# Kernel optimization log

Measured on AMD Instinct MI355X. Metric: run time of the kernel, lower is better.

## Reference

```python
import jax, jax.numpy as jnp
import numpy as np

D_MODEL = 1024
NUM_HEADS = 16
D_K = D_MODEL // NUM_HEADS
MAX_LEN = 1024
BATCH = 8
SEQ = 1024


def setup_inputs() -> dict:
    key = jax.random.key(0)
    ks = jax.random.split(key, 12)
    s = 0.02
    inp = {
        "x": jax.random.normal(ks[0], (BATCH, SEQ, D_MODEL), dtype=jnp.float32),
        "Wq": jax.random.normal(ks[1], (D_MODEL, D_MODEL), dtype=jnp.float32) * s,
        "bq": jnp.zeros((D_MODEL,), dtype=jnp.float32),
        "Wk": jax.random.normal(ks[2], (D_MODEL, D_MODEL), dtype=jnp.float32) * s,
        "bk": jnp.zeros((D_MODEL,), dtype=jnp.float32),
        "Wv": jax.random.normal(ks[3], (D_MODEL, D_MODEL), dtype=jnp.float32) * s,
        "bv": jnp.zeros((D_MODEL,), dtype=jnp.float32),
        "Wo": jax.random.normal(ks[4], (D_MODEL, D_MODEL), dtype=jnp.float32) * s,
        "bo": jnp.zeros((D_MODEL,), dtype=jnp.float32),
        "relative_k": jax.random.normal(ks[5], (2 * MAX_LEN - 1, D_K), dtype=jnp.float32),
        "relative_v": jax.random.normal(ks[6], (2 * MAX_LEN - 1, D_K), dtype=jnp.float32),
    }
    return inp


def reference(x, Wq, bq, Wk, bk, Wv, bv, Wo, bo, relative_k, relative_v):
    B, L, D = x.shape
    H, dk = NUM_HEADS, D_K
    # projections (nn.Linear: y = x @ W.T + b), split into heads -> [B,H,L,dk]
    Q = (x @ Wq.T + bq).reshape(B, L, H, dk).transpose(0, 2, 1, 3)
    K = (x @ Wk.T + bk).reshape(B, L, H, dk).transpose(0, 2, 1, 3)
    V = (x @ Wv.T + bv).reshape(B, L, H, dk).transpose(0, 2, 1, 3)
    # relative position index table: rel_pos[l, r] = r - l + max_len - 1
    rel_pos = jnp.arange(L)[None, :] - jnp.arange(L)[:, None] + (MAX_LEN - 1)
    rel_k = relative_k[rel_pos]  # [L, L, dk]
    rel_v = relative_v[rel_pos]  # [L, L, dk]
    scale = 1.0 / np.sqrt(dk).astype(np.float32)
    scores = jnp.einsum('bhld,bhrd->bhlr', Q, K) * scale
    scores = scores + jnp.einsum('bhld,lrd->bhlr', Q, rel_k)
    attn = jax.nn.softmax(scores, axis=-1)  # [B,H,L,L]
    out = jnp.einsum('bhlr,bhrd->bhld', attn, V)
    out = out + jnp.einsum('bhlr,lrd->bhld', attn, rel_v)
    out = out.transpose(0, 2, 1, 3).reshape(B, L, D)
    return out @ Wo.T + bo
```

## Files before the change

kernel.cpp:

```cpp
#include <hip/hip_runtime.h>

typedef _Float16 f16;
typedef _Float16 f16x2 __attribute__((ext_vector_type(2)));
typedef _Float16 f16x8 __attribute__((ext_vector_type(8)));
typedef float f32x4 __attribute__((ext_vector_type(4)));

static __device__ __forceinline__ f32x4 mfma16(f16x8 a, f16x8 b, f32x4 c) {
  return __builtin_amdgcn_mfma_f32_16x16x32_f16(a, b, c, 0, 0, 0);
}

#define GL16(GP, LP)                                                         \
  __builtin_amdgcn_global_load_lds(                                          \
      (const __attribute__((address_space(1))) void*)(GP),                   \
      (__attribute__((address_space(3))) void*)(LP), 16, 0, 0)

__global__ void pack_f16_kernel(const float* __restrict__ s, f16* __restrict__ d, int n) {
  int i = blockIdx.x * 256 + threadIdx.x;
  if (i < n) d[i] = (f16)s[i];
}

__global__ void pack_relk_kernel(const float* __restrict__ relk, f16* __restrict__ dst) {
  int idx = blockIdx.x * 256 + threadIdx.x;
  dst[idx] = (idx < 2047 * 64) ? (f16)relk[idx] : (f16)0.f;
}

__global__ void pack_relvt_kernel(const float* __restrict__ relv, f16* __restrict__ dst) {
  int idx = blockIdx.x * 256 + threadIdx.x;
  int dd = idx >> 11, p = idx & 2047;
  dst[idx] = (p < 2047) ? (f16)relv[p * 64 + dd] : (f16)0.f;
}

template <int OUT_F32, int BIAS_ROW>
__global__ __launch_bounds__(256, 2) void gemm_bt(
    const f16* __restrict__ A, const f16* __restrict__ B,
    const float* __restrict__ bias, void* __restrict__ Cout,
    int M, int N, int Kd, float oscale) {
  __shared__ __align__(16) f16 Al[2 * 128 * 64];
  __shared__ __align__(16) f16 Bl[2 * 128 * 64];
  const int tid = threadIdx.x;
  const int w = tid >> 6, lane = tid & 63;
  const int l15 = lane & 15, hi = lane >> 4;
  const long i0 = (long)blockIdx.y * 128, j0 = (long)blockIdx.x * 128;
  const int wr = (w >> 1) * 64, wc = (w & 1) * 64;
  const int sx = (l15 & 7) * 8;

  const int row_in = lane >> 3, c_lds = lane & 7;
  const int cg8 = (c_lds ^ row_in) * 8;
  const f16* agl = A + (i0 + w * 8 + row_in) * Kd + cg8;
  const f16* bgl = B + (j0 + w * 8 + row_in) * Kd + cg8;
  const int lbase = (w * 8) * 64;

#define GSTAGE(BUF, K0)                                          \
  do {                                                           \
    f16* al = Al + (BUF) * 8192 + lbase;                         \
    f16* bl = Bl + (BUF) * 8192 + lbase;                         \
    GL16(agl + (K0), al);                                        \
    GL16(agl + 32l * Kd + (K0), al + 32 * 64);                   \
    GL16(agl + 64l * Kd + (K0), al + 64 * 64);                   \
    GL16(agl + 96l * Kd + (K0), al + 96 * 64);                   \
    GL16(bgl + (K0), bl);                                        \
    GL16(bgl + 32l * Kd + (K0), bl + 32 * 64);                   \
    GL16(bgl + 64l * Kd + (K0), bl + 64 * 64);                   \
    GL16(bgl + 96l * Kd + (K0), bl + 96 * 64);                   \
  } while (0)

  f32x4 acc[4][4];
#pragma unroll
  for (int a = 0; a < 4; a++)
#pragma unroll
    for (int b2 = 0; b2 < 4; b2++) acc[a][b2] = (f32x4){0.f, 0.f, 0.f, 0.f};

  GSTAGE(0, 0);
  int cur = 0;
  for (int k0 = 0; k0 < Kd; k0 += 64) {
    if (k0 + 64 < Kd) {
      GSTAGE(cur ^ 1, k0 + 64);
      asm volatile("s_waitcnt vmcnt(8)" ::: "memory");
    } else {
      asm volatile("s_waitcnt vmcnt(0)" ::: "memory");
    }
    __builtin_amdgcn_s_barrier();
    __builtin_amdgcn_sched_barrier(0);
    const f16* Ac = Al + cur * 8192;
    const f16* Bc = Bl + cur * 8192;
#pragma unroll
    for (int ks = 0; ks < 2; ks++) {
      f16x8 af[4], bf[4];
#pragma unroll
      for (int mb = 0; mb < 4; mb++)
        af[mb] = *(const f16x8*)&Ac[(wr + mb * 16 + l15) * 64 + ((ks * 32 + hi * 8) ^ sx)];
#pragma unroll
      for (int nb = 0; nb < 4; nb++)
        bf[nb] = *(const f16x8*)&Bc[(wc + nb * 16 + l15) * 64 + ((ks * 32 + hi * 8) ^ sx)];
#pragma unroll
      for (int mb = 0; mb < 4; mb++)
#pragma unroll
        for (int nb = 0; nb < 4; nb++) acc[mb][nb] = mfma16(af[mb], bf[nb], acc[mb][nb]);
    }
    asm volatile("s_waitcnt lgkmcnt(0)" ::: "memory");
    __builtin_amdgcn_s_barrier();
    cur ^= 1;
  }
#undef GSTAGE
#pragma unroll
  for (int mb = 0; mb < 4; mb++) {
#pragma unroll
    for (int nb = 0; nb < 4; nb++) {
      long row = i0 + wr + mb * 16 + hi * 4;
      long col = j0 + wc + nb * 16 + l15;
      float bc = BIAS_ROW ? 0.f : bias[col];
#pragma unroll
      for (int i = 0; i < 4; i++) {
        float v = acc[mb][nb][i] + (BIAS_ROW ? bias[row + i] : bc);
        v *= oscale;
        if (OUT_F32)
          ((float*)Cout)[(row + i) * N + col] = v;
        else
          ((f16*)Cout)[(row + i) * N + col] = (f16)v;
      }
    }
  }
}

__global__ __launch_bounds__(256, 2) void attn_kernel(
    const f16* __restrict__ Qh, const f16* __restrict__ Kh,
    const f16* __restrict__ Vth, const f16* __restrict__ relKh,
    const f16* __restrict__ relVTh, f16* __restrict__ AO) {
  __shared__ __align__(16) f16 SH[38912];
  f16* const ldsK = SH;
  f16* const ldsRK = SH + 4096;
  f16* const ldsP = SH;
  f16* const ldsPS = SH + 9216;
  f16* const ldsV = SH + 22528;
  f16* const ldsRV = SH + 26624;

  const int tid = threadIdx.x;
  const int w = tid >> 6, lane = tid & 63;
  const int l15 = lane & 15, hi = lane >> 4;
  const int flat = blockIdx.x;
  const int xcd = flat & 7, slot = flat >> 3;
  const int bh = xcd * 16 + (slot >> 3);
  const int qt = slot & 7;
  const int b = bh >> 4, h = bh & 15;
  const int l0 = qt * 128;
  const int cu = 6 - 2 * w;
  const int rvco = 96 - 32 * w;
  const int sx = (l15 & 7) * 8;

  const int row_in = lane >> 3;
  const int c_lds = lane & 7;
  const int cg8 = (c_lds ^ row_in) * 8;
  const f16* kgl = Kh + ((long)(b * 1024 + w * 16 + row_in)) * 1024 + h * 64 + cg8;
  const f16* vgl = Vth + ((long)(h * 64 + w * 16 + row_in)) * 8192 + b * 1024 + cg8;
  const f16* rkgl = relKh + (long)(896 - l0 + w * 48 + row_in) * 64 + cg8;
#define RVP(Q)                                                                   \
  (relVTh + (long)(((w * 6 + (Q)) * 64 + lane) / 24) * 2048 + (896 - l0) +       \
   ((((w * 6 + (Q)) * 64 + lane) % 24) ^ ((((w * 6 + (Q)) * 64 + lane) / 24) & 7)) * 8)
  const f16* rvg0 = RVP(0);
  const f16* rvg1 = RVP(1);
  const f16* rvg2 = RVP(2);
  const f16* rvg3 = RVP(3);
  const f16* rvg4 = RVP(4);
  const f16* rvg5 = RVP(5);
#undef RVP

  const long qbase = ((long)(b * 1024 + l0 + w * 32 + l15)) * 1024 + h * 64 + hi * 8;
  const f16x8 qf00 = *(const f16x8*)(Qh + qbase);
  const f16x8 qf01 = *(const f16x8*)(Qh + qbase + 32);
  const f16x8 qf10 = *(const f16x8*)(Qh + qbase + 16l * 1024);
  const f16x8 qf11 = *(const f16x8*)(Qh + qbase + 16l * 1024 + 32);

  const f16x8 ones1 = {(f16)1.f, (f16)1.f, (f16)1.f, (f16)1.f,
                       (f16)1.f, (f16)1.f, (f16)1.f, (f16)1.f};

  f32x4 acc_o[2][4];
#pragma unroll
  for (int g = 0; g < 2; g++)
#pragma unroll
    for (int cf = 0; cf < 4; cf++) acc_o[g][cf] = (f32x4){0.f, 0.f, 0.f, 0.f};
  float mrow[2][4], lsum[2][4];
#pragma unroll
  for (int g = 0; g < 2; g++)
#pragma unroll
    for (int i = 0; i < 4; i++) {
      mrow[g][i] = -1e30f;
      lsum[g][i] = 0.f;
    }

  for (int kt = 0; kt < 16; kt++) {
    const int r0 = kt * 64;
    __syncthreads();
    {
      const long ko = (long)r0 * 1024;
      GL16(kgl + ko, ldsK + (w * 16) * 64);
      GL16(kgl + ko + 8 * 1024, ldsK + (w * 16 + 8) * 64);
      GL16(vgl + r0, ldsV + (w * 16) * 64);
      GL16(vgl + r0 + 8l * 8192, ldsV + (w * 16 + 8) * 64);
      const int rko = r0 * 64;
      GL16(rkgl + rko, ldsRK + (w * 48) * 64);
      GL16(rkgl + rko + 512, ldsRK + (w * 48 + 8) * 64);
      GL16(rkgl + rko + 1024, ldsRK + (w * 48 + 16) * 64);
      GL16(rkgl + rko + 1536, ldsRK + (w * 48 + 24) * 64);
      GL16(rkgl + rko + 2048, ldsRK + (w * 48 + 32) * 64);
      GL16(rkgl + rko + 2560, ldsRK + (w * 48 + 40) * 64);
      GL16(rvg0 + r0, ldsRV + (w * 6 + 0) * 512);
      GL16(rvg1 + r0, ldsRV + (w * 6 + 1) * 512);
      GL16(rvg2 + r0, ldsRV + (w * 6 + 2) * 512);
      GL16(rvg3 + r0, ldsRV + (w * 6 + 3) * 512);
      GL16(rvg4 + r0, ldsRV + (w * 6 + 4) * 512);
      GL16(rvg5 + r0, ldsRV + (w * 6 + 5) * 512);
    }
    __syncthreads();

    f32x4 sacc[2][4], qracc[2][5];
#pragma unroll
    for (int g = 0; g < 2; g++) {
#pragma unroll
      for (int cf = 0; cf < 4; cf++) sacc[g][cf] = (f32x4){0.f, 0.f, 0.f, 0.f};
#pragma unroll
      for (int j = 0; j < 5; j++) qracc[g][j] = (f32x4){0.f, 0.f, 0.f, 0.f};
    }
    __builtin_amdgcn_s_setprio(1);
#pragma unroll
    for (int ks = 0; ks < 2; ks++) {
      f16x8 kf[4], rf[6];
#pragma unroll
      for (int cf = 0; cf < 4; cf++)
        kf[cf] = *(const f16x8*)&ldsK[(cf * 16 + l15) * 64 + ((ks * 32 + hi * 8) ^ sx)];
#pragma unroll
      for (int j = 0; j < 6; j++)
        rf[j] =
            *(const f16x8*)&ldsRK[((cu + j) * 16 + l15) * 64 + ((ks * 32 + hi * 8) ^ sx)];
      f16x8 q0 = ks ? qf01 : qf00;
      f16x8 q1 = ks ? qf11 : qf10;
#pragma unroll
      for (int cf = 0; cf < 4; cf++) {
        sacc[0][cf] = mfma16(q0, kf[cf], sacc[0][cf]);
        sacc[1][cf] = mfma16(q1, kf[cf], sacc[1][cf]);
      }
#pragma unroll
      for (int j = 0; j < 5; j++) {
        qracc[0][j] = mfma16(q0, rf[j + 1], qracc[0][j]);
        qracc[1][j] = mfma16(q1, rf[j], qracc[1][j]);
      }
    }
    __builtin_amdgcn_s_setprio(0);
    __syncthreads();

#pragma unroll
    for (int g = 0; g < 2; g++)
#pragma unroll
      for (int i = 0; i < 4; i++) {
        int t = 15 + l15 - (hi * 4 + i);
        int idx = (hi * 16 + (t & 15)) * 4;
        bool wrap = t >= 16;
#pragma unroll
        for (int cf = 0; cf < 4; cf++) {
          auto pkv = __builtin_amdgcn_cvt_pkrtz(qracc[g][cf][i], qracc[g][cf + 1][i]);
          int gg = __builtin_amdgcn_ds_bpermute(idx, __builtin_bit_cast(int, pkv));
          f16x2 two = __builtin_bit_cast(f16x2, gg);
          sacc[g][cf][i] += (float)(wrap ? two[1] : two[0]);
        }
      }

    float rmax[2][4];
#pragma unroll
    for (int g = 0; g < 2; g++)
#pragma unroll
      for (int i = 0; i < 4; i++)
        rmax[g][i] = fmaxf(fmaxf(sacc[g][0][i], sacc[g][1][i]),
                           fmaxf(sacc[g][2][i], sacc[g][3][i]));
#pragma unroll
    for (int m = 1; m < 16; m <<= 1)
#pragma unroll
      for (int g = 0; g < 2; g++)
#pragma unroll
        for (int i = 0; i < 4; i++)
          rmax[g][i] = fmaxf(rmax[g][i], __shfl_xor(rmax[g][i], m, 64));
    {
      bool big = false;
#pragma unroll
      for (int g = 0; g < 2; g++)
#pragma unroll
        for (int i = 0; i < 4; i++) big |= rmax[g][i] > mrow[g][i] + 8.f;
      if (__any(big)) {
#pragma unroll
        for (int g = 0; g < 2; g++)
#pragma unroll
          for (int i = 0; i < 4; i++) {
            float mn = fmaxf(mrow[g][i], rmax[g][i]);
            float al = __expf(mrow[g][i] - mn);
            mrow[g][i] = mn;
            lsum[g][i] *= al;
#pragma unroll
            for (int cf = 0; cf < 4; cf++) acc_o[g][cf][i] *= al;
          }
      }
    }
#pragma unroll
    for (int g = 0; g < 2; g++)
#pragma unroll
      for (int cf = 0; cf < 4; cf++)
#pragma unroll
        for (int i = 0; i < 4; i++)
          sacc[g][cf][i] = __expf(sacc[g][cf][i] - mrow[g][i]);

    const uint4 z4 = make_uint4(0u, 0u, 0u, 0u);
#pragma unroll
    for (int r2 = 0; r2 < 2; r2++)
#pragma unroll
      for (int s = 0; s < 3; s++)
        *(uint4*)&ldsPS[(w * 32 + r2 * 16 + (lane >> 2)) * 104 + (lane & 3) * 8 + 32 * s] =
            z4;
#pragma unroll
    for (int g = 0; g < 2; g++)
#pragma unroll
      for (int cf = 0; cf < 4; cf++)
#pragma unroll
        for (int i = 0; i < 4; i++) {
          int rr = 16 * g + hi * 4 + i;
          int ri = cf * 16 + l15;
          f16 ph = (f16)sacc[g][cf][i];
          ldsP[(w * 32 + rr) * 72 + ri] = ph;
          ldsPS[(w * 32 + rr) * 104 + 31 + ri - rr] = ph;
        }
    __builtin_amdgcn_sched_barrier(0);

    __builtin_amdgcn_s_setprio(1);
    f32x4 rs0 = (f32x4){0.f, 0.f, 0.f, 0.f}, rs1 = (f32x4){0.f, 0.f, 0.f, 0.f};
#pragma unroll
    for (int ks = 0; ks < 2; ks++) {
      f16x8 pa0 = *(const f16x8*)&ldsP[(w * 32 + l15) * 72 + ks * 32 + hi * 8];
      f16x8 pa1 = *(const f16x8*)&ldsP[(w * 32 + 16 + l15) * 72 + ks * 32 + hi * 8];
      rs0 = mfma16(pa0, ones1, rs0);
      rs1 = mfma16(pa1, ones1, rs1);
#pragma unroll
      for (int cf = 0; cf < 4; cf++) {
        f16x8 vb = *(const f16x8*)&ldsV[(cf * 16 + l15) * 64 + ((ks * 32 + hi * 8) ^ sx)];
        acc_o[0][cf] = mfma16(pa0, vb, acc_o[0][cf]);
        acc_o[1][cf] = mfma16(pa1, vb, acc_o[1][cf]);
      }
    }
#pragma unroll
    for (int ks = 0; ks < 3; ks++) {
      f16x8 ps0 = *(const f16x8*)&ldsPS[(w * 32 + l15) * 104 + ks * 32 + hi * 8];
      f16x8 ps1 = *(const f16x8*)&ldsPS[(w * 32 + 16 + l15) * 104 + ks * 32 + hi * 8];
#pragma unroll
      for (int cf = 0; cf < 4; cf++) {
        f16x8 rb = *(const f16x8*)&ldsRV[(cf * 16 + l15) * 192 +
                                         ((rvco + ks * 32 + hi * 8) ^ sx)];
        acc_o[0][cf] = mfma16(ps0, rb, acc_o[0][cf]);
        acc_o[1][cf] = mfma16(ps1, rb, acc_o[1][cf]);
      }
    }
    __builtin_amdgcn_s_setprio(0);
#pragma unroll
    for (int i = 0; i < 4; i++) {
      lsum[0][i] += rs0[i];
      lsum[1][i] += rs1[i];
    }
  }
#pragma unroll
  for (int g = 0; g < 2; g++)
#pragma unroll
    for (int cf = 0; cf < 4; cf++)
#pragma unroll
      for (int i = 0; i < 4; i++) {
        float v = acc_o[g][cf][i] / lsum[g][i];
        AO[((long)(b * 1024 + l0 + w * 32 + 16 * g + hi * 4 + i)) * 1024 + h * 64 +
           cf * 16 + l15] = (f16)v;
      }
}

extern "C" void kernel_launch(void* const* d_in, const int* in_sizes, int n_in,
                              void* d_out, int out_size, void* d_ws, size_t ws_size,
                              hipStream_t stream) {
  const float* x = (const float*)d_in[0];
  const float* Wq = (const float*)d_in[1];
  const float* bq = (const float*)d_in[2];
  const float* Wk = (const float*)d_in[3];
  const float* bk = (const float*)d_in[4];
  const float* Wv = (const float*)d_in[5];
  const float* bv = (const float*)d_in[6];
  const float* Wo = (const float*)d_in[7];
  const float* bo = (const float*)d_in[8];
  const float* relk = (const float*)d_in[9];
  const float* relv = (const float*)d_in[10];
  float* out = (float*)d_out;

  char* ws = (char*)d_ws;
  size_t off = 0;
  auto alloc = [&](size_t bytes) {
    char* p = ws + off;
    off += (bytes + 255) & ~(size_t)255;
    return p;
  };
  f16* xh = (f16*)alloc(8192ull * 1024 * 2);
  f16* Wqh = (f16*)alloc(1024ull * 1024 * 2);
  f16* Wkh = (f16*)alloc(1024ull * 1024 * 2);
  f16* Wvh = (f16*)alloc(1024ull * 1024 * 2);
  f16* Woh = (f16*)alloc(1024ull * 1024 * 2);
  f16* relKh = (f16*)alloc(2048ull * 64 * 2);
  f16* relVTh = (f16*)alloc(64ull * 2048 * 2);
  f16* Qh = (f16*)alloc(8192ull * 1024 * 2);
  f16* Kh = (f16*)alloc(8192ull * 1024 * 2);
  f16* Vth = (f16*)alloc(1024ull * 8192 * 2);
  f16* AOh = (f16*)alloc(8192ull * 1024 * 2);
  if (ws_size < off) return;

  pack_f16_kernel<<<32768, 256, 0, stream>>>(x, xh, 8192 * 1024);
  pack_f16_kernel<<<4096, 256, 0, stream>>>(Wq, Wqh, 1024 * 1024);
  pack_f16_kernel<<<4096, 256, 0, stream>>>(Wk, Wkh, 1024 * 1024);
  pack_f16_kernel<<<4096, 256, 0, stream>>>(Wv, Wvh, 1024 * 1024);
  pack_f16_kernel<<<4096, 256, 0, stream>>>(Wo, Woh, 1024 * 1024);
  pack_relk_kernel<<<512, 256, 0, stream>>>(relk, relKh);
  pack_relvt_kernel<<<512, 256, 0, stream>>>(relv, relVTh);

  dim3 g1(8, 64);
  gemm_bt<0, 0><<<g1, 256, 0, stream>>>(xh, Wqh, bq, Qh, 8192, 1024, 1024, 1.0f);
  gemm_bt<0, 0><<<g1, 256, 0, stream>>>(xh, Wkh, bk, Kh, 8192, 1024, 1024, 0.125f);
  dim3 g2(64, 8);
  gemm_bt<0, 1><<<g2, 256, 0, stream>>>(Wvh, xh, bv, Vth, 1024, 8192, 1024, 1.0f);

  attn_kernel<<<1024, 256, 0, stream>>>(Qh, Kh, Vth, relKh, relVTh, AOh);

  gemm_bt<1, 0><<<g1, 256, 0, stream>>>(AOh, Woh, bo, out, 8192, 1024, 1024, 1.0f);
}
```

Measured before the change: 300.1 us.

## Fuse pack kernels, batch Q/K GEMMs, and split attention load wait

Merges the five f32-to-f16 pack launches into one vectorized float4 kernel and the two relative-table packs into one kernel. Batches the Q and K projections into a single GEMM launch using blockIdx.z to select weights, bias, output and scale. In the attention loop, V and relative-V loads are issued last and a partial vmcnt wait replaces the full __syncthreads, so the QK stage can start while those loads are still in flight. This cuts launch count and tail effects and overlaps memory with compute, but relies on hand-counted vmcnt ordering being correct.

```diff
diff --git a/kernel.cpp b/kernel.cpp
--- a/kernel.cpp
+++ b/kernel.cpp
@@ -2,6 +2,7 @@
 
 typedef _Float16 f16;
 typedef _Float16 f16x2 __attribute__((ext_vector_type(2)));
+typedef _Float16 f16x4 __attribute__((ext_vector_type(4)));
 typedef _Float16 f16x8 __attribute__((ext_vector_type(8)));
 typedef float f32x4 __attribute__((ext_vector_type(4)));
 
@@ -14,27 +15,55 @@
       (const __attribute__((address_space(1))) void*)(GP),                   \
       (__attribute__((address_space(3))) void*)(LP), 16, 0, 0)
 
-__global__ void pack_f16_kernel(const float* __restrict__ s, f16* __restrict__ d, int n) {
+__global__ void pack5_kernel(const float4* __restrict__ x, const float4* __restrict__ wq,
+                             const float4* __restrict__ wk, const float4* __restrict__ wv,
+                             const float4* __restrict__ wo, f16* __restrict__ xh,
+                             f16* __restrict__ wqh, f16* __restrict__ wkh,
+                             f16* __restrict__ wvh, f16* __restrict__ woh) {
   int i = blockIdx.x * 256 + threadIdx.x;
-  if (i < n) d[i] = (f16)s[i];
-}
-
-__global__ void pack_relk_kernel(const float* __restrict__ relk, f16* __restrict__ dst) {
+  const float4* s;
+  f16* d;
+  int off;
+  if (i < 2097152) {
+    s = x;
+    d = xh;
+    off = i;
+  } else {
+    int j = i - 2097152;
+    int seg = j >> 18;
+    off = j & 262143;
+    s = seg == 0 ? wq : seg == 1 ? wk : seg == 2 ? wv : wo;
+    d = seg == 0 ? wqh : seg == 1 ? wkh : seg == 2 ? wvh : woh;
+  }
+  float4 v = s[off];
+  f16x4 o = {(f16)v.x, (f16)v.y, (f16)v.z, (f16)v.w};
+  *(f16x4*)&d[off * 4] = o;
+}
+
+__global__ void packrel_kernel(const float* __restrict__ relk,
+                               const float* __restrict__ relv,
+                               f16* __restrict__ relKh, f16* __restrict__ relVTh) {
   int idx = blockIdx.x * 256 + threadIdx.x;
-  dst[idx] = (idx < 2047 * 64) ? (f16)relk[idx] : (f16)0.f;
-}
-
-__global__ void pack_relvt_kernel(const float* __restrict__ relv, f16* __restrict__ dst) {
-  int idx = blockIdx.x * 256 + threadIdx.x;
-  int dd = idx >> 11, p = idx & 2047;
-  dst[idx] = (p < 2047) ? (f16)relv[p * 64 + dd] : (f16)0.f;
+  if (idx < 131072) {
+    relKh[idx] = (idx < 2047 * 64) ? (f16)relk[idx] : (f16)0.f;
+  } else {
+    int k = idx - 131072;
+    int dd = k >> 11, p = k & 2047;
+    relVTh[k] = (p < 2047) ? (f16)relv[p * 64 + dd] : (f16)0.f;
+  }
 }
 
 template <int OUT_F32, int BIAS_ROW>
 __global__ __launch_bounds__(256, 2) void gemm_bt(
-    const f16* __restrict__ A, const f16* __restrict__ B,
-    const float* __restrict__ bias, void* __restrict__ Cout,
-    int M, int N, int Kd, float oscale) {
+    const f16* __restrict__ A, const f16* __restrict__ Bp0, const f16* __restrict__ Bp1,
+    const float* __restrict__ bias0, const float* __restrict__ bias1,
+    void* __restrict__ C0, void* __restrict__ C1,
+    int M, int N, int Kd, float osc0, float osc1) {
+  const f16* B = blockIdx.z ? Bp1 : Bp0;
+  const float* bias = blockIdx.z ? bias1 : bias0;
+  void* Cout = blockIdx.z ? C1 : C0;
+  const float oscale = blockIdx.z ? osc1 : osc0;
+
   __shared__ __align__(16) f16 Al[2 * 128 * 64];
   __shared__ __align__(16) f16 Bl[2 * 128 * 64];
   const int tid = threadIdx.x;
@@ -194,8 +223,6 @@
       const long ko = (long)r0 * 1024;
       GL16(kgl + ko, ldsK + (w * 16) * 64);
       GL16(kgl + ko + 8 * 1024, ldsK + (w * 16 + 8) * 64);
-      GL16(vgl + r0, ldsV + (w * 16) * 64);
-      GL16(vgl + r0 + 8l * 8192, ldsV + (w * 16 + 8) * 64);
       const int rko = r0 * 64;
       GL16(rkgl + rko, ldsRK + (w * 48) * 64);
       GL16(rkgl + rko + 512, ldsRK + (w * 48 + 8) * 64);
@@ -203,6 +230,8 @@
       GL16(rkgl + rko + 1536, ldsRK + (w * 48 + 24) * 64);
       GL16(rkgl + rko + 2048, ldsRK + (w * 48 + 32) * 64);
       GL16(rkgl + rko + 2560, ldsRK + (w * 48 + 40) * 64);
+      GL16(vgl + r0, ldsV + (w * 16) * 64);
+      GL16(vgl + r0 + 8l * 8192, ldsV + (w * 16 + 8) * 64);
       GL16(rvg0 + r0, ldsRV + (w * 6 + 0) * 512);
       GL16(rvg1 + r0, ldsRV + (w * 6 + 1) * 512);
       GL16(rvg2 + r0, ldsRV + (w * 6 + 2) * 512);
@@ -210,7 +239,9 @@
       GL16(rvg4 + r0, ldsRV + (w * 6 + 4) * 512);
       GL16(rvg5 + r0, ldsRV + (w * 6 + 5) * 512);
     }
-    __syncthreads();
+    asm volatile("s_waitcnt vmcnt(8)" ::: "memory");
+    __builtin_amdgcn_s_barrier();
+    __builtin_amdgcn_sched_barrier(0);
 
     f32x4 sacc[2][4], qracc[2][5];
 #pragma unroll
@@ -408,21 +439,18 @@
   f16* AOh = (f16*)alloc(8192ull * 1024 * 2);
   if (ws_size < off) return;
 
-  pack_f16_kernel<<<32768, 256, 0, stream>>>(x, xh, 8192 * 1024);
-  pack_f16_kernel<<<4096, 256, 0, stream>>>(Wq, Wqh, 1024 * 1024);
-  pack_f16_kernel<<<4096, 256, 0, stream>>>(Wk, Wkh, 1024 * 1024);
-  pack_f16_kernel<<<4096, 256, 0, stream>>>(Wv, Wvh, 1024 * 1024);
-  pack_f16_kernel<<<4096, 256, 0, stream>>>(Wo, Woh, 1024 * 1024);
-  pack_relk_kernel<<<512, 256, 0, stream>>>(relk, relKh);
-  pack_relvt_kernel<<<512, 256, 0, stream>>>(relv, relVTh);
-
-  dim3 g1(8, 64);
-  gemm_bt<0, 0><<<g1, 256, 0, stream>>>(xh, Wqh, bq, Qh, 8192, 1024, 1024, 1.0f);
-  gemm_bt<0, 0><<<g1, 256, 0, stream>>>(xh, Wkh, bk, Kh, 8192, 1024, 1024, 0.125f);
-  dim3 g2(64, 8);
-  gemm_bt<0, 1><<<g2, 256, 0, stream>>>(Wvh, xh, bv, Vth, 1024, 8192, 1024, 1.0f);
+  pack5_kernel<<<12288, 256, 0, stream>>>((const float4*)x, (const float4*)Wq,
+                                          (const float4*)Wk, (const float4*)Wv,
+                                          (const float4*)Wo, xh, Wqh, Wkh, Wvh, Woh);
+  packrel_kernel<<<1024, 256, 0, stream>>>(relk, relv, relKh, relVTh);
+
+  gemm_bt<0, 0><<<dim3(8, 64, 2), 256, 0, stream>>>(
+      xh, Wqh, Wkh, bq, bk, Qh, Kh, 8192, 1024, 1024, 1.0f, 0.125f);
+  gemm_bt<0, 1><<<dim3(64, 8, 1), 256, 0, stream>>>(
+      Wvh, xh, xh, bv, bv, Vth, Vth, 1024, 8192, 1024, 1.0f, 1.0f);
 
   attn_kernel<<<1024, 256, 0, stream>>>(Qh, Kh, Vth, relKh, relVTh, AOh);
 
-  gemm_bt<1, 0><<<g1, 256, 0, stream>>>(AOh, Woh, bo, out, 8192, 1024, 1024, 1.0f);
-}
+  gemm_bt<1, 0><<<dim3(8, 64, 1), 256, 0, stream>>>(
+      AOh, Woh, Woh, bo, bo, out, out, 8192, 1024, 1024, 1.0f, 1.0f);
+}
```

New measurement: 286.5 us. -4.5%, faster.
